# Performance work log

Measured on AMD Instinct MI355X. Metric: run time of the kernel, lower is better.

## Reference

```python
import jax, jax.numpy as jnp
import numpy as np

N, E = 100000, 1600000
IN_DIM, HID, NCLS = 64, 128, 18
BATCH, K = 8, 5000


def setup_inputs() -> dict:
    key = jax.random.key(0)
    ks = jax.random.split(key, 9)
    features = jax.random.normal(ks[0], (N, IN_DIM), dtype=jnp.float32)
    src = jax.random.randint(ks[1], (E,), 0, N, dtype=jnp.int32)
    dst = jax.random.randint(ks[2], (E,), 0, N, dtype=jnp.int32)
    def glorot(k, shape):
        lim = float(np.sqrt(6.0 / (shape[0] + shape[1])))
        return jax.random.uniform(k, shape, jnp.float32, -lim, lim)
    W1 = glorot(ks[3], (IN_DIM, HID)); b1 = jnp.zeros((HID,), jnp.float32)
    W2 = glorot(ks[4], (HID, HID));    b2 = jnp.zeros((HID,), jnp.float32)
    W3 = glorot(ks[5], (K * HID, NCLS)); b3 = jnp.zeros((NCLS,), jnp.float32)
    return {"features": features, "src": src, "dst": dst,
            "W1": W1, "b1": b1, "W2": W2, "b2": b2, "W3": W3, "b3": b3}


def reference(features, src, dst, W1, b1, W2, b2, W3, b3):
    n = features.shape[0]
    ones = jnp.ones(src.shape[0], features.dtype)
    out_deg = jax.ops.segment_sum(ones, src, num_segments=n)
    in_deg = jax.ops.segment_sum(ones, dst, num_segments=n)
    norm_src = jnp.clip(out_deg, 1.0) ** -0.5  # DGL norm='both'
    norm_dst = jnp.clip(in_deg, 1.0) ** -0.5

    def gconv(x, W, b, act):
        h = (x @ W) * norm_src[:, None]          # transform then normalize src
        agg = jax.ops.segment_sum(h[src], dst, num_segments=n)  # gather+scatter-add
        agg = agg * norm_dst[:, None] + b
        return jax.nn.relu(agg) if act else agg

    h = gconv(features, W1, b1, True)   # [N, HID]
    h = gconv(h, W2, b2, True)          # [N, HID]

    # global_sort_pool: equal-sized graphs of N//BATCH nodes, top-K by last channel
    n_per = n // BATCH
    hb = h.reshape(BATCH, n_per, HID)
    _, idx = jax.lax.top_k(hb[..., -1], K)                  # [B, K] descending
    topk = jnp.take_along_axis(hb, idx[..., None], axis=1)  # [B, K, HID]
    pooled = topk.reshape(BATCH, K * HID)

    return pooled @ W3 + b3  # [B, NCLS]
```

## Files before the change

### kernel.cpp

```cpp
#include <hip/hip_runtime.h>
#include <cstdint>
#include <cstddef>

#define N_NODES 100000
#define N_EDGES 1600000
#define IN_DIM  64
#define HID     128
#define NCLS    18
#define BATCH   8
#define TOPK    5000
#define NPER    12500
#define SORTN   16384
#define SORTC   2048

#define BSHIFT  9
#define BNODES  (1 << BSHIFT)
#define NBUCK   ((N_NODES + BNODES - 1) / BNODES)
#define CHUNK   8192


__global__ __launch_bounds__(256) void k_bcount(const int* __restrict__ src,
                                                const int* __restrict__ dst,
                                                int* __restrict__ bcntS,
                                                int* __restrict__ bcntD) {
    __shared__ int cs[NBUCK], cd[NBUCK];
    for (int b = threadIdx.x; b < NBUCK; b += 256) { cs[b] = 0; cd[b] = 0; }
    __syncthreads();
    const int base = blockIdx.x * CHUNK;
    const int end  = min(base + CHUNK, N_EDGES);
    for (int e = base + threadIdx.x; e < end; e += 256) {
        atomicAdd(&cs[src[e] >> BSHIFT], 1);
        atomicAdd(&cd[dst[e] >> BSHIFT], 1);
    }
    __syncthreads();
    for (int b = threadIdx.x; b < NBUCK; b += 256) {
        if (cs[b]) atomicAdd(&bcntS[b], cs[b]);
        if (cd[b]) atomicAdd(&bcntD[b], cd[b]);
    }
}

__global__ void k_bscan(const int* __restrict__ bcntS, const int* __restrict__ bcntD,
                        int* __restrict__ baseS, int* __restrict__ baseD,
                        int* __restrict__ curS, int* __restrict__ curD) {
    if (threadIdx.x == 0 && blockIdx.x == 0) {
        int rs = 0, rd = 0;
        for (int b = 0; b < NBUCK; ++b) {
            baseS[b] = rs; curS[b] = rs; rs += bcntS[b];
            baseD[b] = rd; curD[b] = rd; rd += bcntD[b];
        }
        baseS[NBUCK] = rs; baseD[NBUCK] = rd;
    }
}


__global__ __launch_bounds__(256) void k_bin(const int* __restrict__ src,
                                             const int* __restrict__ dst,
                                             int* __restrict__ cursorD,
                                             unsigned* __restrict__ binbuf) {
    __shared__ int cnt[NBUCK];
    __shared__ int gbase[NBUCK];
    __shared__ int cnt2[NBUCK];
    const int base = blockIdx.x * CHUNK;
    const int end  = min(base + CHUNK, N_EDGES);
    for (int b = threadIdx.x; b < NBUCK; b += 256) { cnt[b] = 0; cnt2[b] = 0; }
    __syncthreads();
    for (int e = base + threadIdx.x; e < end; e += 256)
        atomicAdd(&cnt[dst[e] >> BSHIFT], 1);
    __syncthreads();
    for (int b = threadIdx.x; b < NBUCK; b += 256)
        if (cnt[b] > 0) gbase[b] = atomicAdd(&cursorD[b], cnt[b]);
    __syncthreads();
    for (int e = base + threadIdx.x; e < end; e += 256) {
        int d = dst[e];
        int b = d >> BSHIFT;
        int off = atomicAdd(&cnt2[b], 1);
        unsigned packed = ((unsigned)(d & (BNODES - 1)) << 17) | (unsigned)src[e];
        binbuf[gbase[b] + off] = packed;
    }
}

__global__ __launch_bounds__(256) void k_bin_src(const int* __restrict__ src,
                                                 int* __restrict__ cursorS,
                                                 unsigned* __restrict__ sbin) {
    __shared__ int cnt[NBUCK];
    __shared__ int gbase[NBUCK];
    __shared__ int cnt2[NBUCK];
    const int base = blockIdx.x * CHUNK;
    const int end  = min(base + CHUNK, N_EDGES);
    for (int b = threadIdx.x; b < NBUCK; b += 256) { cnt[b] = 0; cnt2[b] = 0; }
    __syncthreads();
    for (int e = base + threadIdx.x; e < end; e += 256)
        atomicAdd(&cnt[src[e] >> BSHIFT], 1);
    __syncthreads();
    for (int b = threadIdx.x; b < NBUCK; b += 256)
        if (cnt[b] > 0) gbase[b] = atomicAdd(&cursorS[b], cnt[b]);
    __syncthreads();
    for (int e = base + threadIdx.x; e < end; e += 256) {
        int s = src[e];
        int b = s >> BSHIFT;
        int off = atomicAdd(&cnt2[b], 1);
        sbin[gbase[b] + off] = (unsigned)(s & (BNODES - 1));
    }
}


__global__ __launch_bounds__(256) void k_histS(const unsigned* __restrict__ sbin,
                                               const int* __restrict__ baseS,
                                               float* __restrict__ normS) {
    __shared__ int cnt[BNODES];
    for (int t = threadIdx.x; t < BNODES; t += 256) cnt[t] = 0;
    __syncthreads();
    const int beg = baseS[blockIdx.x], end = baseS[blockIdx.x + 1];
    for (int e = beg + threadIdx.x; e < end; e += 256)
        atomicAdd(&cnt[sbin[e]], 1);
    __syncthreads();
    const int nodeBase = blockIdx.x << BSHIFT;
    for (int t = threadIdx.x; t < BNODES; t += 256) {
        int node = nodeBase + t;
        if (node < N_NODES)
            normS[node] = 1.0f / sqrtf((float)max(cnt[t], 1));
    }
}

__global__ __launch_bounds__(256) void k_histD_scatter(const unsigned* __restrict__ binbuf,
                                                       const int* __restrict__ baseD,
                                                       float* __restrict__ normD,
                                                       int* __restrict__ row_ptr,
                                                       int* __restrict__ ssrc) {
    __shared__ int cnt[BNODES];
    __shared__ int tmp[BNODES];
    for (int t = threadIdx.x; t < BNODES; t += 256) cnt[t] = 0;
    __syncthreads();
    const int beg = baseD[blockIdx.x], end = baseD[blockIdx.x + 1];
    for (int e = beg + threadIdx.x; e < end; e += 256)
        atomicAdd(&cnt[binbuf[e] >> 17], 1);
    __syncthreads();
    const int nodeBase = blockIdx.x << BSHIFT;
    for (int t = threadIdx.x; t < BNODES; t += 256) {
        int node = nodeBase + t;
        if (node < N_NODES)
            normD[node] = 1.0f / sqrtf((float)max(cnt[t], 1));
    }
    for (int s = 1; s < BNODES; s <<= 1) {
        for (int t = threadIdx.x; t < BNODES; t += 256)
            tmp[t] = (t >= s) ? cnt[t - s] + cnt[t] : cnt[t];
        __syncthreads();
        for (int t = threadIdx.x; t < BNODES; t += 256) cnt[t] = tmp[t];
        __syncthreads();
    }
    for (int t = threadIdx.x; t < BNODES; t += 256) {
        int b = beg + ((t == 0) ? 0 : cnt[t - 1]);
        tmp[t] = b;
        int node = nodeBase + t;
        if (node < N_NODES) row_ptr[node] = b;
    }
    if (blockIdx.x == 0 && threadIdx.x == 0) row_ptr[N_NODES] = N_EDGES;
    __syncthreads();
    for (int e = beg + threadIdx.x; e < end; e += 256) {
        unsigned v = binbuf[e];
        int pos = atomicAdd(&tmp[v >> 17], 1);
        ssrc[pos] = (int)(v & 0x1FFFFu);
    }
}


__global__ __launch_bounds__(256) void k_agg64(const float* __restrict__ hs,
                                               const int* __restrict__ row_ptr,
                                               const int* __restrict__ ssrc,
                                               const float* __restrict__ normS,
                                               float* __restrict__ out) {
    const int node = blockIdx.x * 16 + (threadIdx.x >> 4);
    const int lane = threadIdx.x & 15;
    if (node >= N_NODES) return;
    const int beg = row_ptr[node], end = row_ptr[node + 1];
    const float4* __restrict__ hv = (const float4*)hs;
    float4 acc = make_float4(0.f, 0.f, 0.f, 0.f);
    int e = beg;
    for (; e + 4 <= end; e += 4) {
        int s0 = ssrc[e + 0], s1 = ssrc[e + 1], s2 = ssrc[e + 2], s3 = ssrc[e + 3];
        float n0 = normS[s0], n1 = normS[s1], n2 = normS[s2], n3 = normS[s3];
        float4 v0 = hv[(size_t)s0 * 16 + lane];
        float4 v1 = hv[(size_t)s1 * 16 + lane];
        float4 v2 = hv[(size_t)s2 * 16 + lane];
        float4 v3 = hv[(size_t)s3 * 16 + lane];
        acc.x += v0.x * n0; acc.y += v0.y * n0; acc.z += v0.z * n0; acc.w += v0.w * n0;
        acc.x += v1.x * n1; acc.y += v1.y * n1; acc.z += v1.z * n1; acc.w += v1.w * n1;
        acc.x += v2.x * n2; acc.y += v2.y * n2; acc.z += v2.z * n2; acc.w += v2.w * n2;
        acc.x += v3.x * n3; acc.y += v3.y * n3; acc.z += v3.z * n3; acc.w += v3.w * n3;
    }
    for (; e < end; ++e) {
        int s0 = ssrc[e];
        float n0 = normS[s0];
        float4 v0 = hv[(size_t)s0 * 16 + lane];
        acc.x += v0.x * n0; acc.y += v0.y * n0; acc.z += v0.z * n0; acc.w += v0.w * n0;
    }
    *(float4*)(out + (size_t)node * IN_DIM + lane * 4) = acc;
}

#define ACC4(A, V) { A.x += V.x; A.y += V.y; A.z += V.z; A.w += V.w; }

__global__ __launch_bounds__(256) void k_agg128(const float* __restrict__ hs,
                                                const int* __restrict__ row_ptr,
                                                const int* __restrict__ ssrc,
                                                float* __restrict__ out) {
    const int node = blockIdx.x * 8 + (threadIdx.x >> 5);
    const int lane = threadIdx.x & 31;
    if (node >= N_NODES) return;
    const int beg = row_ptr[node], end = row_ptr[node + 1];
    const float4* __restrict__ hv = (const float4*)hs;
    float4 acc = make_float4(0.f, 0.f, 0.f, 0.f);
    int e = beg;
    for (; e + 4 <= end; e += 4) {
        int s0 = ssrc[e + 0], s1 = ssrc[e + 1], s2 = ssrc[e + 2], s3 = ssrc[e + 3];
        float4 v0 = hv[(size_t)s0 * 32 + lane];
        float4 v1 = hv[(size_t)s1 * 32 + lane];
        float4 v2 = hv[(size_t)s2 * 32 + lane];
        float4 v3 = hv[(size_t)s3 * 32 + lane];
        ACC4(acc, v0); ACC4(acc, v1); ACC4(acc, v2); ACC4(acc, v3);
    }
    for (; e < end; ++e) {
        float4 v0 = hv[(size_t)ssrc[e] * 32 + lane];
        ACC4(acc, v0);
    }
    *(float4*)(out + (size_t)node * HID + lane * 4) = acc;
}


#define BMT 64
#define BKT 32

template<int KDIM, bool POST, bool KEYS>
__global__ __launch_bounds__(256) void k_gemm_rt(const float* __restrict__ X,
                                                 const float* __restrict__ W,
                                                 const float* __restrict__ normD,
                                                 const float* __restrict__ bias,
                                                 const float* __restrict__ normS,
                                                 float* __restrict__ keys,
                                                 float* __restrict__ out) {
    __shared__ float xs[BMT][BKT + 4];
    __shared__ float ws[BKT * HID];

    const int tid = threadIdx.x;
    const int tx = tid & 31;
    const int ty = tid >> 5;
    const int col0 = tx * 4;
    const int row0 = ty * 8;
    const int rt = blockIdx.x * BMT;

    float acc[8][4];
    #pragma unroll
    for (int r = 0; r < 8; ++r)
        #pragma unroll
        for (int c = 0; c < 4; ++c) acc[r][c] = 0.f;

    for (int k0 = 0; k0 < KDIM; k0 += BKT) {
        __syncthreads();
        {
            const float4* wsrc = (const float4*)(W + (size_t)k0 * HID);
            #pragma unroll
            for (int i = tid; i < BKT * HID / 4; i += 256)
                ((float4*)ws)[i] = wsrc[i];
        }
        {
            #pragma unroll
            for (int i = tid; i < BMT * BKT / 4; i += 256) {
                int row = i >> 3;
                int kq  = i & 7;
                int gr  = rt + row;
                float4 v = make_float4(0.f, 0.f, 0.f, 0.f);
                if (gr < N_NODES)
                    v = *(const float4*)(X + (size_t)gr * KDIM + k0 + kq * 4);
                *(float4*)&xs[row][kq * 4] = v;
            }
        }
        __syncthreads();

        #pragma unroll 4
        for (int k = 0; k < BKT; ++k) {
            float4 b = *(const float4*)&ws[k * HID + col0];
            float a[8];
            #pragma unroll
            for (int r = 0; r < 8; ++r) a[r] = xs[row0 + r][k];
            #pragma unroll
            for (int r = 0; r < 8; ++r) {
                acc[r][0] += a[r] * b.x;
                acc[r][1] += a[r] * b.y;
                acc[r][2] += a[r] * b.z;
                acc[r][3] += a[r] * b.w;
            }
        }
    }

    const float4 bb = *(const float4*)(bias + col0);
    #pragma unroll
    for (int r = 0; r < 8; ++r) {
        int gr = rt + row0 + r;
        if (gr < N_NODES) {
            float nd = normD[gr];
            float4 o;
            o.x = fmaxf(acc[r][0] * nd + bb.x, 0.f);
            o.y = fmaxf(acc[r][1] * nd + bb.y, 0.f);
            o.z = fmaxf(acc[r][2] * nd + bb.z, 0.f);
            o.w = fmaxf(acc[r][3] * nd + bb.w, 0.f);
            if (KEYS && col0 == 124) keys[gr] = o.w;
            if (POST) {
                float ns = normS[gr];
                o.x *= ns; o.y *= ns; o.z *= ns; o.w *= ns;
            }
            *(float4*)(out + (size_t)gr * HID + col0) = o;
        }
    }
}


__global__ __launch_bounds__(256) void k_sort_init(const float* __restrict__ keys,
                                                   unsigned long long* __restrict__ arr) {
    int i = blockIdx.x * 256 + threadIdx.x;
    if (i >= BATCH * SORTN) return;
    int g = i >> 14;
    int l = i & (SORTN - 1);
    unsigned long long c;
    if (l < NPER) {
        unsigned u = __float_as_uint(keys[g * NPER + l]);
        unsigned s = (u & 0x80000000u) ? ~u : (u | 0x80000000u);
        unsigned d = ~s;
        c = ((unsigned long long)d << 32) | (unsigned)l;
    } else {
        c = 0xFFFFFFFFFFFFFFFFull;
    }
    arr[i] = c;
}

__global__ __launch_bounds__(1024) void k_sort_local_full(unsigned long long* __restrict__ arr) {
    __shared__ unsigned long long lds[SORTC];
    const int base  = blockIdx.x * SORTC;
    const int gbase = base & (SORTN - 1);
    lds[threadIdx.x]        = arr[base + threadIdx.x];
    lds[threadIdx.x + 1024] = arr[base + threadIdx.x + 1024];
    __syncthreads();
    for (int k = 2; k <= SORTC; k <<= 1) {
        for (int j = k >> 1; j > 0; j >>= 1) {
            int t = threadIdx.x;
            int i = ((t & ~(j - 1)) << 1) | (t & (j - 1));
            bool up = (((gbase + i) & k) == 0);
            unsigned long long a = lds[i], b = lds[i + j];
            if ((a > b) == up) { lds[i] = b; lds[i + j] = a; }
            __syncthreads();
        }
    }
    arr[base + threadIdx.x]        = lds[threadIdx.x];
    arr[base + threadIdx.x + 1024] = lds[threadIdx.x + 1024];
}

__global__ __launch_bounds__(256) void k_sort_global(unsigned long long* __restrict__ arr,
                                                     int k, int j) {
    int tg = blockIdx.x * 256 + threadIdx.x;
    if (tg >= BATCH * (SORTN / 2)) return;
    int g = tg >> 13;
    int t = tg & (SORTN / 2 - 1);
    int i = ((t & ~(j - 1)) << 1) | (t & (j - 1));
    bool up = ((i & k) == 0);
    unsigned long long* p = arr + (size_t)g * SORTN;
    unsigned long long a = p[i], b = p[i + j];
    if ((a > b) == up) { p[i] = b; p[i + j] = a; }
}

__global__ __launch_bounds__(1024) void k_sort_local_tail(unsigned long long* __restrict__ arr,
                                                          int k) {
    __shared__ unsigned long long lds[SORTC];
    const int base  = blockIdx.x * SORTC;
    const int gbase = base & (SORTN - 1);
    lds[threadIdx.x]        = arr[base + threadIdx.x];
    lds[threadIdx.x + 1024] = arr[base + threadIdx.x + 1024];
    __syncthreads();
    for (int j = SORTC >> 1; j > 0; j >>= 1) {
        int t = threadIdx.x;
        int i = ((t & ~(j - 1)) << 1) | (t & (j - 1));
        bool up = (((gbase + i) & k) == 0);
        unsigned long long a = lds[i], b = lds[i + j];
        if ((a > b) == up) { lds[i] = b; lds[i + j] = a; }
        __syncthreads();
    }
    arr[base + threadIdx.x]        = lds[threadIdx.x];
    arr[base + threadIdx.x + 1024] = lds[threadIdx.x + 1024];
}

__global__ __launch_bounds__(256) void k_sort_emit(const unsigned long long* __restrict__ arr,
                                                   int* __restrict__ topk_idx) {
    int i = blockIdx.x * 256 + threadIdx.x;
    if (i >= BATCH * TOPK) return;
    int b = i / TOPK;
    int k = i - b * TOPK;
    topk_idx[i] = (int)(arr[(size_t)b * SORTN + k] & 0xFFFFFFFFull);
}


__global__ void k_outinit(const float* __restrict__ b3, float* __restrict__ out) {
    int i = threadIdx.x;
    if (i < BATCH * NCLS) out[i] = b3[i % NCLS];
}

#define KPB 100

__global__ __launch_bounds__(128) void k_final(const float* __restrict__ h2,
                                               const int* __restrict__ topk_idx,
                                               const float* __restrict__ W3,
                                               float* __restrict__ out) {
    __shared__ float red[128 * NCLS];
    const int b = blockIdx.x / (TOPK / KPB);
    const int chunk = blockIdx.x % (TOPK / KPB);
    const int j = threadIdx.x;
    float acc[NCLS];
    #pragma unroll
    for (int c = 0; c < NCLS; ++c) acc[c] = 0.f;
    const int k0 = chunk * KPB;
    for (int k = k0; k < k0 + KPB; ++k) {
        int node = b * NPER + topk_idx[b * TOPK + k];
        float h = h2[(size_t)node * HID + j];
        const float* wrow = W3 + (size_t)(k * HID + j) * NCLS;
        #pragma unroll
        for (int c = 0; c < NCLS; ++c) acc[c] += h * wrow[c];
    }
    #pragma unroll
    for (int c = 0; c < NCLS; ++c) red[j * NCLS + c] = acc[c];
    __syncthreads();
    for (int s = 64; s > 0; s >>= 1) {
        if (j < s) {
            #pragma unroll
            for (int c = 0; c < NCLS; ++c) red[j * NCLS + c] += red[(j + s) * NCLS + c];
        }
        __syncthreads();
    }
    if (j < NCLS) atomicAdd(&out[b * NCLS + j], red[j]);
}


extern "C" void kernel_launch(void* const* d_in, const int* in_sizes, int n_in,
                              void* d_out, int out_size, void* d_ws, size_t ws_size,
                              hipStream_t stream) {
    const float* features = (const float*)d_in[0];
    const int*   src      = (const int*)d_in[1];
    const int*   dst      = (const int*)d_in[2];
    const float* W1       = (const float*)d_in[3];
    const float* b1       = (const float*)d_in[4];
    const float* W2       = (const float*)d_in[5];
    const float* b2       = (const float*)d_in[6];
    const float* W3       = (const float*)d_in[7];
    const float* b3       = (const float*)d_in[8];
    float* out = (float*)d_out;

    char* p = (char*)d_ws;
    auto carve = [&](size_t bytes) -> void* {
        void* r = (void*)p;
        p += (bytes + 511) & ~(size_t)511;
        return r;
    };
    float* normS     = (float*)carve((size_t)N_NODES * 4);
    float* normD     = (float*)carve((size_t)N_NODES * 4);
    int*   row_ptr   = (int*)carve((size_t)(N_NODES + 1) * 4);
    int*   bcntS     = (int*)carve((size_t)NBUCK * 4);
    int*   bcntD     = (int*)carve((size_t)NBUCK * 4);
    int*   baseS     = (int*)carve((size_t)(NBUCK + 1) * 4);
    int*   baseD     = (int*)carve((size_t)(NBUCK + 1) * 4);
    int*   curS      = (int*)carve((size_t)NBUCK * 4);
    int*   curD      = (int*)carve((size_t)NBUCK * 4);
    int*   ssrc      = (int*)carve((size_t)N_EDGES * 4);
    unsigned* binbuf = (unsigned*)carve((size_t)N_EDGES * 4);
    unsigned* sbin   = (unsigned*)carve((size_t)N_EDGES * 4);
    float* keys      = (float*)carve((size_t)N_NODES * 4);
    int*   topk_idx  = (int*)carve((size_t)BATCH * TOPK * 4);
    unsigned long long* sortbuf = (unsigned long long*)carve((size_t)BATCH * SORTN * 8);
    float* bufA      = (float*)carve((size_t)N_NODES * HID * 4);
    float* bufB      = (float*)carve((size_t)N_NODES * HID * 4);
    float* g1        = (float*)carve((size_t)N_NODES * IN_DIM * 4);

    const int GB = (N_NODES + BMT - 1) / BMT;
    const int BB = (N_EDGES + CHUNK - 1) / CHUNK;

    hipMemsetAsync(bcntS, 0, (size_t)NBUCK * 4, stream);
    hipMemsetAsync(bcntD, 0, (size_t)NBUCK * 4, stream);

    k_bcount<<<BB, 256, 0, stream>>>(src, dst, bcntS, bcntD);
    k_bscan<<<1, 64, 0, stream>>>(bcntS, bcntD, baseS, baseD, curS, curD);
    k_bin<<<BB, 256, 0, stream>>>(src, dst, curD, binbuf);
    k_bin_src<<<BB, 256, 0, stream>>>(src, curS, sbin);
    k_histS<<<NBUCK, 256, 0, stream>>>(sbin, baseS, normS);
    k_histD_scatter<<<NBUCK, 256, 0, stream>>>(binbuf, baseD, normD, row_ptr, ssrc);

    k_agg64<<<(N_NODES + 15) / 16, 256, 0, stream>>>(features, row_ptr, ssrc, normS, g1);
    k_gemm_rt<IN_DIM, true, false><<<GB, 256, 0, stream>>>(g1, W1, normD, b1, normS, nullptr, bufA);
    k_agg128<<<(N_NODES + 7) / 8, 256, 0, stream>>>(bufA, row_ptr, ssrc, bufB);
    k_gemm_rt<HID, false, true><<<GB, 256, 0, stream>>>(bufB, W2, normD, b2, nullptr, keys, bufA);

    const int NCHUNK = BATCH * SORTN / SORTC;
    const int GCE    = (BATCH * (SORTN / 2) + 255) / 256;
    k_sort_init<<<(BATCH * SORTN + 255) / 256, 256, 0, stream>>>(keys, sortbuf);
    k_sort_local_full<<<NCHUNK, 1024, 0, stream>>>(sortbuf);
    k_sort_global<<<GCE, 256, 0, stream>>>(sortbuf, 4096, 2048);
    k_sort_local_tail<<<NCHUNK, 1024, 0, stream>>>(sortbuf, 4096);
    k_sort_global<<<GCE, 256, 0, stream>>>(sortbuf, 8192, 4096);
    k_sort_global<<<GCE, 256, 0, stream>>>(sortbuf, 8192, 2048);
    k_sort_local_tail<<<NCHUNK, 1024, 0, stream>>>(sortbuf, 8192);
    k_sort_global<<<GCE, 256, 0, stream>>>(sortbuf, 16384, 8192);
    k_sort_global<<<GCE, 256, 0, stream>>>(sortbuf, 16384, 4096);
    k_sort_global<<<GCE, 256, 0, stream>>>(sortbuf, 16384, 2048);
    k_sort_local_tail<<<NCHUNK, 1024, 0, stream>>>(sortbuf, 16384);
    k_sort_emit<<<(BATCH * TOPK + 255) / 256, 256, 0, stream>>>(sortbuf, topk_idx);

    k_outinit<<<1, 256, 0, stream>>>(b3, out);
    k_final<<<BATCH * (TOPK / KPB), 128, 0, stream>>>(bufA, topk_idx, W3, out);
}
```

Measured before the change: 594.7 us.

## Fuse aggregation into GEMM kernels and merge binning/histogram kernels

Neighbor aggregation is now done inside the GEMM kernel, which writes the aggregated rows straight into shared memory so the intermediate g1 and bufB round trips through global memory go away. The dst and src binning kernels are merged into one, as are the two histogram kernels. The output bias init is folded into the sort-emit kernel. Together these cut kernel launches and global traffic, but the GEMM blocks now do irregular gather work and use more shared memory (a 64x132 tile), which may lower occupancy and overlap.

```diff
diff --git a/kernel.cpp b/kernel.cpp
--- a/kernel.cpp
+++ b/kernel.cpp
@@ -53,89 +53,72 @@
 }
 
 
-__global__ __launch_bounds__(256) void k_bin(const int* __restrict__ src,
-                                             const int* __restrict__ dst,
-                                             int* __restrict__ cursorD,
-                                             unsigned* __restrict__ binbuf) {
-    __shared__ int cnt[NBUCK];
-    __shared__ int gbase[NBUCK];
-    __shared__ int cnt2[NBUCK];
+__global__ __launch_bounds__(256) void k_bin2(const int* __restrict__ src,
+                                              const int* __restrict__ dst,
+                                              int* __restrict__ cursorD,
+                                              int* __restrict__ cursorS,
+                                              unsigned* __restrict__ binbuf,
+                                              unsigned* __restrict__ sbin) {
+    __shared__ int cD[NBUCK], gD[NBUCK], aD[NBUCK];
+    __shared__ int cS[NBUCK], gS[NBUCK], aS[NBUCK];
     const int base = blockIdx.x * CHUNK;
     const int end  = min(base + CHUNK, N_EDGES);
-    for (int b = threadIdx.x; b < NBUCK; b += 256) { cnt[b] = 0; cnt2[b] = 0; }
-    __syncthreads();
-    for (int e = base + threadIdx.x; e < end; e += 256)
-        atomicAdd(&cnt[dst[e] >> BSHIFT], 1);
-    __syncthreads();
-    for (int b = threadIdx.x; b < NBUCK; b += 256)
-        if (cnt[b] > 0) gbase[b] = atomicAdd(&cursorD[b], cnt[b]);
+    for (int b = threadIdx.x; b < NBUCK; b += 256) {
+        cD[b] = 0; aD[b] = 0; cS[b] = 0; aS[b] = 0;
+    }
     __syncthreads();
     for (int e = base + threadIdx.x; e < end; e += 256) {
-        int d = dst[e];
-        int b = d >> BSHIFT;
-        int off = atomicAdd(&cnt2[b], 1);
-        unsigned packed = ((unsigned)(d & (BNODES - 1)) << 17) | (unsigned)src[e];
-        binbuf[gbase[b] + off] = packed;
-    }
-}
-
-__global__ __launch_bounds__(256) void k_bin_src(const int* __restrict__ src,
-                                                 int* __restrict__ cursorS,
-                                                 unsigned* __restrict__ sbin) {
-    __shared__ int cnt[NBUCK];
-    __shared__ int gbase[NBUCK];
-    __shared__ int cnt2[NBUCK];
-    const int base = blockIdx.x * CHUNK;
-    const int end  = min(base + CHUNK, N_EDGES);
-    for (int b = threadIdx.x; b < NBUCK; b += 256) { cnt[b] = 0; cnt2[b] = 0; }
-    __syncthreads();
-    for (int e = base + threadIdx.x; e < end; e += 256)
-        atomicAdd(&cnt[src[e] >> BSHIFT], 1);
-    __syncthreads();
-    for (int b = threadIdx.x; b < NBUCK; b += 256)
-        if (cnt[b] > 0) gbase[b] = atomicAdd(&cursorS[b], cnt[b]);
+        atomicAdd(&cD[dst[e] >> BSHIFT], 1);
+        atomicAdd(&cS[src[e] >> BSHIFT], 1);
+    }
+    __syncthreads();
+    for (int b = threadIdx.x; b < NBUCK; b += 256) {
+        if (cD[b] > 0) gD[b] = atomicAdd(&cursorD[b], cD[b]);
+        if (cS[b] > 0) gS[b] = atomicAdd(&cursorS[b], cS[b]);
+    }
     __syncthreads();
     for (int e = base + threadIdx.x; e < end; e += 256) {
-        int s = src[e];
-        int b = s >> BSHIFT;
-        int off = atomicAdd(&cnt2[b], 1);
-        sbin[gbase[b] + off] = (unsigned)(s & (BNODES - 1));
-    }
-}
-
-
-__global__ __launch_bounds__(256) void k_histS(const unsigned* __restrict__ sbin,
-                                               const int* __restrict__ baseS,
-                                               float* __restrict__ normS) {
+        int d = dst[e], s = src[e];
+        int bd = d >> BSHIFT;
+        int od = atomicAdd(&aD[bd], 1);
+        binbuf[gD[bd] + od] = ((unsigned)(d & (BNODES - 1)) << 17) | (unsigned)s;
+        int bs = s >> BSHIFT;
+        int os = atomicAdd(&aS[bs], 1);
+        sbin[gS[bs] + os] = (unsigned)(s & (BNODES - 1));
+    }
+}
+
+
+__global__ __launch_bounds__(256) void k_hist_all(const unsigned* __restrict__ sbin,
+                                                  const int* __restrict__ baseS,
+                                                  const unsigned* __restrict__ binbuf,
+                                                  const int* __restrict__ baseD,
+                                                  float* __restrict__ normS,
+                                                  float* __restrict__ normD,
+                                                  int* __restrict__ row_ptr,
+                                                  int* __restrict__ ssrc) {
     __shared__ int cnt[BNODES];
+    __shared__ int tmp[BNODES];
+    const int nodeBase = blockIdx.x << BSHIFT;
     for (int t = threadIdx.x; t < BNODES; t += 256) cnt[t] = 0;
     __syncthreads();
-    const int beg = baseS[blockIdx.x], end = baseS[blockIdx.x + 1];
-    for (int e = beg + threadIdx.x; e < end; e += 256)
-        atomicAdd(&cnt[sbin[e]], 1);
-    __syncthreads();
-    const int nodeBase = blockIdx.x << BSHIFT;
+    {
+        const int beg = baseS[blockIdx.x], end = baseS[blockIdx.x + 1];
+        for (int e = beg + threadIdx.x; e < end; e += 256)
+            atomicAdd(&cnt[sbin[e]], 1);
+    }
+    __syncthreads();
     for (int t = threadIdx.x; t < BNODES; t += 256) {
         int node = nodeBase + t;
         if (node < N_NODES)
             normS[node] = 1.0f / sqrtf((float)max(cnt[t], 1));
-    }
-}
-
-__global__ __launch_bounds__(256) void k_histD_scatter(const unsigned* __restrict__ binbuf,
-                                                       const int* __restrict__ baseD,
-                                                       float* __restrict__ normD,
-                                                       int* __restrict__ row_ptr,
-                                                       int* __restrict__ ssrc) {
-    __shared__ int cnt[BNODES];
-    __shared__ int tmp[BNODES];
-    for (int t = threadIdx.x; t < BNODES; t += 256) cnt[t] = 0;
+        cnt[t] = 0;
+    }
     __syncthreads();
     const int beg = baseD[blockIdx.x], end = baseD[blockIdx.x + 1];
     for (int e = beg + threadIdx.x; e < end; e += 256)
         atomicAdd(&cnt[binbuf[e] >> 17], 1);
     __syncthreads();
-    const int nodeBase = blockIdx.x << BSHIFT;
     for (int t = threadIdx.x; t < BNODES; t += 256) {
         int node = nodeBase + t;
         if (node < N_NODES)
@@ -164,88 +147,78 @@
 }
 
 
-__global__ __launch_bounds__(256) void k_agg64(const float* __restrict__ hs,
+#define BMT 64
+#define BKT 32
+
+template<int KDIM, bool SCALE, bool POST, bool KEYS>
+__global__ __launch_bounds__(256) void k_fused(const float* __restrict__ X,
                                                const int* __restrict__ row_ptr,
                                                const int* __restrict__ ssrc,
-                                               const float* __restrict__ normS,
+                                               const float* __restrict__ normSrc,
+                                               const float* __restrict__ W,
+                                               const float* __restrict__ normD,
+                                               const float* __restrict__ bias,
+                                               const float* __restrict__ normS_post,
+                                               float* __restrict__ keys,
                                                float* __restrict__ out) {
-    const int node = blockIdx.x * 16 + (threadIdx.x >> 4);
-    const int lane = threadIdx.x & 15;
-    if (node >= N_NODES) return;
-    const int beg = row_ptr[node], end = row_ptr[node + 1];
-    const float4* __restrict__ hv = (const float4*)hs;
-    float4 acc = make_float4(0.f, 0.f, 0.f, 0.f);
-    int e = beg;
-    for (; e + 4 <= end; e += 4) {
-        int s0 = ssrc[e + 0], s1 = ssrc[e + 1], s2 = ssrc[e + 2], s3 = ssrc[e + 3];
-        float n0 = normS[s0], n1 = normS[s1], n2 = normS[s2], n3 = normS[s3];
-        float4 v0 = hv[(size_t)s0 * 16 + lane];
-        float4 v1 = hv[(size_t)s1 * 16 + lane];
-        float4 v2 = hv[(size_t)s2 * 16 + lane];
-        float4 v3 = hv[(size_t)s3 * 16 + lane];
-        acc.x += v0.x * n0; acc.y += v0.y * n0; acc.z += v0.z * n0; acc.w += v0.w * n0;
-        acc.x += v1.x * n1; acc.y += v1.y * n1; acc.z += v1.z * n1; acc.w += v1.w * n1;
-        acc.x += v2.x * n2; acc.y += v2.y * n2; acc.z += v2.z * n2; acc.w += v2.w * n2;
-        acc.x += v3.x * n3; acc.y += v3.y * n3; acc.z += v3.z * n3; acc.w += v3.w * n3;
-    }
-    for (; e < end; ++e) {
-        int s0 = ssrc[e];
-        float n0 = normS[s0];
-        float4 v0 = hv[(size_t)s0 * 16 + lane];
-        acc.x += v0.x * n0; acc.y += v0.y * n0; acc.z += v0.z * n0; acc.w += v0.w * n0;
-    }
-    *(float4*)(out + (size_t)node * IN_DIM + lane * 4) = acc;
-}
-
-#define ACC4(A, V) { A.x += V.x; A.y += V.y; A.z += V.z; A.w += V.w; }
-
-__global__ __launch_bounds__(256) void k_agg128(const float* __restrict__ hs,
-                                                const int* __restrict__ row_ptr,
-                                                const int* __restrict__ ssrc,
-                                                float* __restrict__ out) {
-    const int node = blockIdx.x * 8 + (threadIdx.x >> 5);
-    const int lane = threadIdx.x & 31;
-    if (node >= N_NODES) return;
-    const int beg = row_ptr[node], end = row_ptr[node + 1];
-    const float4* __restrict__ hv = (const float4*)hs;
-    float4 acc = make_float4(0.f, 0.f, 0.f, 0.f);
-    int e = beg;
-    for (; e + 4 <= end; e += 4) {
-        int s0 = ssrc[e + 0], s1 = ssrc[e + 1], s2 = ssrc[e + 2], s3 = ssrc[e + 3];
-        float4 v0 = hv[(size_t)s0 * 32 + lane];
-        float4 v1 = hv[(size_t)s1 * 32 + lane];
-        float4 v2 = hv[(size_t)s2 * 32 + lane];
-        float4 v3 = hv[(size_t)s3 * 32 + lane];
-        ACC4(acc, v0); ACC4(acc, v1); ACC4(acc, v2); ACC4(acc, v3);
-    }
-    for (; e < end; ++e) {
-        float4 v0 = hv[(size_t)ssrc[e] * 32 + lane];
-        ACC4(acc, v0);
-    }
-    *(float4*)(out + (size_t)node * HID + lane * 4) = acc;
-}
-
-
-#define BMT 64
-#define BKT 32
-
-template<int KDIM, bool POST, bool KEYS>
-__global__ __launch_bounds__(256) void k_gemm_rt(const float* __restrict__ X,
-                                                 const float* __restrict__ W,
-                                                 const float* __restrict__ normD,
-                                                 const float* __restrict__ bias,
-                                                 const float* __restrict__ normS,
-                                                 float* __restrict__ keys,
-                                                 float* __restrict__ out) {
-    __shared__ float xs[BMT][BKT + 4];
+    __shared__ float xs[BMT][KDIM + 4];
     __shared__ float ws[BKT * HID];
 
     const int tid = threadIdx.x;
+    const int rt = blockIdx.x * BMT;
+
+    {
+        constexpr int LPN = KDIM / 4;
+        constexpr int NCH = 256 / LPN;
+        const int w = tid / LPN;
+        const int lane = tid % LPN;
+        const float4* __restrict__ hv = (const float4*)X;
+        #pragma unroll
+        for (int c = 0; c < BMT / NCH; ++c) {
+            const int row = c * NCH + w;
+            const int node = rt + row;
+            float4 a4 = make_float4(0.f, 0.f, 0.f, 0.f);
+            if (node < N_NODES) {
+                const int beg = row_ptr[node], end = row_ptr[node + 1];
+                int e = beg;
+                for (; e + 4 <= end; e += 4) {
+                    int s0 = ssrc[e + 0], s1 = ssrc[e + 1], s2 = ssrc[e + 2], s3 = ssrc[e + 3];
+                    float4 v0 = hv[(size_t)s0 * LPN + lane];
+                    float4 v1 = hv[(size_t)s1 * LPN + lane];
+                    float4 v2 = hv[(size_t)s2 * LPN + lane];
+                    float4 v3 = hv[(size_t)s3 * LPN + lane];
+                    if constexpr (SCALE) {
+                        float n0 = normSrc[s0], n1 = normSrc[s1], n2 = normSrc[s2], n3 = normSrc[s3];
+                        a4.x += v0.x * n0; a4.y += v0.y * n0; a4.z += v0.z * n0; a4.w += v0.w * n0;
+                        a4.x += v1.x * n1; a4.y += v1.y * n1; a4.z += v1.z * n1; a4.w += v1.w * n1;
+                        a4.x += v2.x * n2; a4.y += v2.y * n2; a4.z += v2.z * n2; a4.w += v2.w * n2;
+                        a4.x += v3.x * n3; a4.y += v3.y * n3; a4.z += v3.z * n3; a4.w += v3.w * n3;
+                    } else {
+                        a4.x += v0.x; a4.y += v0.y; a4.z += v0.z; a4.w += v0.w;
+                        a4.x += v1.x; a4.y += v1.y; a4.z += v1.z; a4.w += v1.w;
+                        a4.x += v2.x; a4.y += v2.y; a4.z += v2.z; a4.w += v2.w;
+                        a4.x += v3.x; a4.y += v3.y; a4.z += v3.z; a4.w += v3.w;
+                    }
+                }
+                for (; e < end; ++e) {
+                    int s0 = ssrc[e];
+                    float4 v0 = hv[(size_t)s0 * LPN + lane];
+                    if constexpr (SCALE) {
+                        float n0 = normSrc[s0];
+                        a4.x += v0.x * n0; a4.y += v0.y * n0; a4.z += v0.z * n0; a4.w += v0.w * n0;
+                    } else {
+                        a4.x += v0.x; a4.y += v0.y; a4.z += v0.z; a4.w += v0.w;
+                    }
+                }
+            }
+            *(float4*)&xs[row][lane * 4] = a4;
+        }
+    }
+
     const int tx = tid & 31;
     const int ty = tid >> 5;
     const int col0 = tx * 4;
     const int row0 = ty * 8;
-    const int rt = blockIdx.x * BMT;
 
     float acc[8][4];
     #pragma unroll
@@ -261,26 +234,13 @@
             for (int i = tid; i < BKT * HID / 4; i += 256)
                 ((float4*)ws)[i] = wsrc[i];
         }
-        {
-            #pragma unroll
-            for (int i = tid; i < BMT * BKT / 4; i += 256) {
-                int row = i >> 3;
-                int kq  = i & 7;
-                int gr  = rt + row;
-                float4 v = make_float4(0.f, 0.f, 0.f, 0.f);
-                if (gr < N_NODES)
-                    v = *(const float4*)(X + (size_t)gr * KDIM + k0 + kq * 4);
-                *(float4*)&xs[row][kq * 4] = v;
-            }
-        }
-        __syncthreads();
-
+        __syncthreads();
         #pragma unroll 4
         for (int k = 0; k < BKT; ++k) {
             float4 b = *(const float4*)&ws[k * HID + col0];
             float a[8];
             #pragma unroll
-            for (int r = 0; r < 8; ++r) a[r] = xs[row0 + r][k];
+            for (int r = 0; r < 8; ++r) a[r] = xs[row0 + r][k0 + k];
             #pragma unroll
             for (int r = 0; r < 8; ++r) {
                 acc[r][0] += a[r] * b.x;
@@ -304,7 +264,7 @@
             o.w = fmaxf(acc[r][3] * nd + bb.w, 0.f);
             if (KEYS && col0 == 124) keys[gr] = o.w;
             if (POST) {
-                float ns = normS[gr];
+                float ns = normS_post[gr];
                 o.x *= ns; o.y *= ns; o.z *= ns; o.w *= ns;
             }
             *(float4*)(out + (size_t)gr * HID + col0) = o;
@@ -386,19 +346,17 @@
 }
 
 __global__ __launch_bounds__(256) void k_sort_emit(const unsigned long long* __restrict__ arr,
-                                                   int* __restrict__ topk_idx) {
+                                                   int* __restrict__ topk_idx,
+                                                   const float* __restrict__ b3,
+                                                   float* __restrict__ out) {
     int i = blockIdx.x * 256 + threadIdx.x;
+    if (i < BATCH * NCLS) out[i] = b3[i % NCLS];
     if (i >= BATCH * TOPK) return;
     int b = i / TOPK;
     int k = i - b * TOPK;
     topk_idx[i] = (int)(arr[(size_t)b * SORTN + k] & 0xFFFFFFFFull);
 }
 
-
-__global__ void k_outinit(const float* __restrict__ b3, float* __restrict__ out) {
-    int i = threadIdx.x;
-    if (i < BATCH * NCLS) out[i] = b3[i % NCLS];
-}
 
 #define KPB 100
 
@@ -472,7 +430,6 @@
     unsigned long long* sortbuf = (unsigned long long*)carve((size_t)BATCH * SORTN * 8);
     float* bufA      = (float*)carve((size_t)N_NODES * HID * 4);
     float* bufB      = (float*)carve((size_t)N_NODES * HID * 4);
-    float* g1        = (float*)carve((size_t)N_NODES * IN_DIM * 4);
 
     const int GB = (N_NODES + BMT - 1) / BMT;
     const int BB = (N_EDGES + CHUNK - 1) / CHUNK;
@@ -482,15 +439,14 @@
 
     k_bcount<<<BB, 256, 0, stream>>>(src, dst, bcntS, bcntD);
     k_bscan<<<1, 64, 0, stream>>>(bcntS, bcntD, baseS, baseD, curS, curD);
-    k_bin<<<BB, 256, 0, stream>>>(src, dst, curD, binbuf);
-    k_bin_src<<<BB, 256, 0, stream>>>(src, curS, sbin);
-    k_histS<<<NBUCK, 256, 0, stream>>>(sbin, baseS, normS);
-    k_histD_scatter<<<NBUCK, 256, 0, stream>>>(binbuf, baseD, normD, row_ptr, ssrc);
-
-    k_agg64<<<(N_NODES + 15) / 16, 256, 0, stream>>>(features, row_ptr, ssrc, normS, g1);
-    k_gemm_rt<IN_DIM, true, false><<<GB, 256, 0, stream>>>(g1, W1, normD, b1, normS, nullptr, bufA);
-    k_agg128<<<(N_NODES + 7) / 8, 256, 0, stream>>>(bufA, row_ptr, ssrc, bufB);
-    k_gemm_rt<HID, false, true><<<GB, 256, 0, stream>>>(bufB, W2, normD, b2, nullptr, keys, bufA);
+    k_bin2<<<BB, 256, 0, stream>>>(src, dst, curD, curS, binbuf, sbin);
+    k_hist_all<<<NBUCK, 256, 0, stream>>>(sbin, baseS, binbuf, baseD,
+                                          normS, normD, row_ptr, ssrc);
+
+    k_fused<IN_DIM, true, true, false><<<GB, 256, 0, stream>>>(
+        features, row_ptr, ssrc, normS, W1, normD, b1, normS, nullptr, bufA);
+    k_fused<HID, false, false, true><<<GB, 256, 0, stream>>>(
+        bufA, row_ptr, ssrc, nullptr, W2, normD, b2, nullptr, keys, bufB);
 
     const int NCHUNK = BATCH * SORTN / SORTC;
     const int GCE    = (BATCH * (SORTN / 2) + 255) / 256;
@@ -505,8 +461,7 @@
     k_sort_global<<<GCE, 256, 0, stream>>>(sortbuf, 16384, 4096);
     k_sort_global<<<GCE, 256, 0, stream>>>(sortbuf, 16384, 2048);
     k_sort_local_tail<<<NCHUNK, 1024, 0, stream>>>(sortbuf, 16384);
-    k_sort_emit<<<(BATCH * TOPK + 255) / 256, 256, 0, stream>>>(sortbuf, topk_idx);
-
-    k_outinit<<<1, 256, 0, stream>>>(b3, out);
-    k_final<<<BATCH * (TOPK / KPB), 128, 0, stream>>>(bufA, topk_idx, W3, out);
-}
+    k_sort_emit<<<(BATCH * TOPK + 255) / 256, 256, 0, stream>>>(sortbuf, topk_idx, b3, out);
+
+    k_final<<<BATCH * (TOPK / KPB), 128, 0, stream>>>(bufB, topk_idx, W3, out);
+}
```

New measurement: 583.6 us. Within noise of the previous version (-1.9%).
